# Optimization experiments

Hardware: AMD Instinct MI355X
Metric: run time of the kernel (lower is better)

The kernel has to match this reference:

```python
import jax, jax.numpy as jnp
import numpy as np


def _ln(x, g, b, eps=1e-6):
    m = jnp.mean(x, axis=-1, keepdims=True)
    v = jnp.mean((x - m) ** 2, axis=-1, keepdims=True)
    return g * (x - m) * jax.lax.rsqrt(v + eps) + b


def setup_inputs() -> dict:
    key = jax.random.key(0)
    ks = jax.random.split(key, 18)
    B, T, F, K = 4, 2048, 128, 1          # batch, seq, raw features, time2vec kernel size
    D = F * (K + 2)                        # 384 = d_model after time2vec concat
    H, HS, FF = 8, 128, 512                # heads, head_size, ff_dim
    s = 0.02
    inp = {
        "x":    jax.random.normal(ks[0], (B, T, F), jnp.float32),
        # Time2Vec params
        "wb":   jax.random.uniform(ks[1], (F,), jnp.float32, -0.05, 0.05),
        "bb":   jax.random.uniform(ks[2], (F,), jnp.float32, -0.05, 0.05),
        "wa":   jax.random.uniform(ks[3], (F, K), jnp.float32, -0.05, 0.05),
        "ba":   jax.random.uniform(ks[4], (F, K), jnp.float32, -0.05, 0.05),
        # MHA params (per-head kernels, as in the addons layer)
        "Wq":   jax.random.normal(ks[5], (H, D, HS), jnp.float32) * s,
        "Wk":   jax.random.normal(ks[6], (H, D, HS), jnp.float32) * s,
        "Wv":   jax.random.normal(ks[7], (H, D, HS), jnp.float32) * s,
        "Wp":   jax.random.normal(ks[8], (H, HS, D), jnp.float32) * s,
        "bp":   jnp.zeros((D,), jnp.float32),
        "ln1_g": jnp.ones((D,), jnp.float32),
        "ln1_b": jnp.zeros((D,), jnp.float32),
        # FFN (Conv1D kernel_size=1 == dense over channels)
        "W1":   jax.random.normal(ks[9], (D, FF), jnp.float32) * s,
        "b1":   jnp.zeros((FF,), jnp.float32),
        "W2":   jax.random.normal(ks[10], (FF, D), jnp.float32) * s,
        "b2":   jnp.zeros((D,), jnp.float32),
        "ln2_g": jnp.ones((D,), jnp.float32),
        "ln2_b": jnp.zeros((D,), jnp.float32),
    }
    return inp


def reference(x, wb, bb, wa, ba, Wq, Wk, Wv, Wp, bp, ln1_g, ln1_b,
              W1, b1, W2, b2, ln2_g, ln2_b):
    B, T, F = x.shape
    # ---- Time2Vec (applied per timestep) ----
    bias = wb * x + bb                                        # [B,T,F]
    dp = jnp.einsum('btf,fk->btk', x, wa)[:, :, None, :] + ba # [B,T,F,K]
    wgts = jnp.sin(dp)
    t2v = jnp.concatenate([bias[..., None], wgts], axis=-1).reshape(B, T, -1)
    h = jnp.concatenate([x, t2v], axis=-1)                    # [B,T,D]

    # ---- MultiHeadAttention (self-attention, eval: dropout=0) ----
    HS = Wq.shape[-1]
    q = jnp.einsum('bni,hio->bnho', h, Wq) / jnp.sqrt(jnp.asarray(HS, h.dtype))
    k = jnp.einsum('bmi,hio->bmho', h, Wk)
    v = jnp.einsum('bmi,hio->bmho', h, Wv)
    logits = jnp.einsum('bnho,bmho->bhnm', q, k)              # [B,H,T,T]
    attn = jax.nn.softmax(logits, axis=-1)
    mo = jnp.einsum('bhnm,bmhi->bnhi', attn, v)               # [B,T,H,HS]
    a = jnp.einsum('bnhi,hio->bno', mo, Wp) + bp              # [B,T,D]

    h1 = _ln(h + a, ln1_g, ln1_b)
    # ---- FFN (Conv1D ks=1 -> dense) ----
    f = jax.nn.relu(jnp.einsum('btd,df->btf', h1, W1) + b1)
    f = jnp.einsum('btf,fd->btd', f, W2) + b2
    h2 = _ln(h1 + f, ln2_g, ln2_b)

    return h2.reshape(B, -1)                                  # [B, T*D]
```

## Files before the change

### kernel.cpp

```cpp
#include <hip/hip_runtime.h>
#include <hip/hip_bf16.h>

typedef __hip_bfloat16 bf16;
typedef __attribute__((ext_vector_type(8))) short short8;
typedef __attribute__((ext_vector_type(4))) short short4v;
typedef __attribute__((ext_vector_type(4))) float floatx4;

#define B_  4
#define T_  2048
#define F_  128
#define D_  384
#define H_  8
#define HS_ 128
#define FF_ 512
#define NT_ (B_*T_)

__device__ __forceinline__ float b2f(bf16 v) { return __bfloat162float(v); }
__device__ __forceinline__ bf16  f2b(float v) { return __float2bfloat16(v); }
__device__ __forceinline__ unsigned short f2bu(float f) {
    bf16 b = __float2bfloat16(f);
    union { bf16 h; unsigned short u; } cv; cv.h = b; return cv.u;
}

__device__ __forceinline__ float ldin(const void* p, size_t i, int f32) {
    return f32 ? ((const float*)p)[i] : b2f(((const bf16*)p)[i]);
}

__global__ void k_detect(const void* __restrict__ x, int* __restrict__ flag)
{
    if (threadIdx.x == 0 && blockIdx.x == 0) {
        const unsigned short* u = (const unsigned short*)x;
        int big = 0;
        for (int i = 0; i < 128; i++) {
            int e = (u[i] >> 7) & 0xFF;
            if (e >= 141) big++;
        }
        *flag = (big >= 8) ? 1 : 0;
    }
}

__global__ void k_pack_all(const void* __restrict__ Wq, const void* __restrict__ Wk,
                           const void* __restrict__ Wv, const void* __restrict__ Wp,
                           const void* __restrict__ bp, const void* __restrict__ W1,
                           const void* __restrict__ b1, const void* __restrict__ W2,
                           const void* __restrict__ b2, bf16* __restrict__ wbase,
                           const int* __restrict__ dtf, int mode1)
{
    const int f32 = *dtf;
    int idx = blockIdx.x * 256 + threadIdx.x;
    if (idx < 1179648) {
        int k = idx % D_;
        int head, mat, ch;
        if (mode1) {
            int n = idx / D_;
            mat = n >> 10; int w = n & 1023; head = w >> 7; ch = w & 127;
        } else {
            int n = (idx / D_) % 1536; int rnd = idx / (D_ * 1536);
            mat = n >> 9; int w = n & 511; head = rnd * 4 + (w >> 7); ch = w & 127;
        }
        const void* W = (mat == 0 ? Wq : (mat == 1 ? Wk : Wv));
        float v = ldin(W, (size_t)head * D_ * HS_ + (size_t)k * HS_ + ch, f32);
        if (mat == 0) v *= 0.08838834764831845f;
        wbase[idx] = f2b(v);
    } else if (idx < 1572864) {
        int l = idx - 1179648; int o = l >> 10, c = l & 1023;
        wbase[idx] = f2b(ldin(Wp, (size_t)c * D_ + o, f32));
    } else if (idx < 1769472) {
        int l = idx - 1572864; int d = l % D_, f = l / D_;
        wbase[idx] = f2b(ldin(W1, (size_t)d * FF_ + f, f32));
    } else if (idx < 1966080) {
        int l = idx - 1769472; int ff = l % FF_, d = l / FF_;
        wbase[idx] = f2b(ldin(W2, (size_t)ff * D_ + d, f32));
    } else if (idx < 1968896) {
        int l = idx - 1966080;
        float bv = 0.f;
        if (l >= 2432)      bv = ldin(b2, l - 2432, f32);
        else if (l >= 1920) bv = ldin(b1, l - 1920, f32);
        else if (l >= 1536) bv = ldin(bp, l - 1536, f32);
        wbase[idx] = f2b(bv);
    }
}

__global__ void k_t2v(const void* __restrict__ x, const void* __restrict__ wb,
                      const void* __restrict__ bb, const void* __restrict__ wa,
                      const void* __restrict__ ba, bf16* __restrict__ h,
                      const int* __restrict__ dtf)
{
    const int f32 = *dtf;
    int row = blockIdx.x;
    int f = threadIdx.x;
    float xv = ldin(x, (size_t)row * F_ + f, f32);
    float prod = xv * ldin(wa, f, f32);
    #pragma unroll
    for (int off = 32; off; off >>= 1) prod += __shfl_down(prod, off, 64);
    __shared__ float sdot[2];
    if ((threadIdx.x & 63) == 0) sdot[threadIdx.x >> 6] = prod;
    __syncthreads();
    float dot = sdot[0] + sdot[1];

    float bias = ldin(wb, f, f32) * xv + ldin(bb, f, f32);
    float sn   = sinf(dot + ldin(ba, f, f32));
    bf16* hr = h + (size_t)row * D_;
    hr[f]            = f2b(xv);
    hr[F_ + 2*f]     = f2b(bias);
    hr[F_ + 2*f + 1] = f2b(sn);
}

template<bool BIAS, bool RELU>
__global__ __launch_bounds__(256) void
k_gemm_mfma(const bf16* __restrict__ A, const bf16* __restrict__ Wt,
            const bf16* __restrict__ bias, bf16* __restrict__ C,
            int K, int N)
{
    __shared__ __align__(16) bf16 As[128][72];
    __shared__ __align__(16) bf16 Bs[128][72];

    const int tid  = threadIdx.x;
    const int wave = tid >> 6;
    const int lane = tid & 63;
    const int r    = lane & 15;
    const int g    = lane >> 4;
    const int rh   = (wave & 1) * 64;
    const int chh  = (wave >> 1) * 64;
    const int row0 = blockIdx.x * 128;
    const int col0 = blockIdx.y * 128;

    floatx4 acc[4][4];
    #pragma unroll
    for (int mt = 0; mt < 4; mt++)
        #pragma unroll
        for (int nt = 0; nt < 4; nt++) acc[mt][nt] = (floatx4){0.f,0.f,0.f,0.f};

    for (int k0 = 0; k0 < K; k0 += 64) {
        #pragma unroll
        for (int s = 0; s < 4; s++) {
            int i = tid + s * 256;
            int row = i >> 3, c8 = i & 7;
            *(uint4*)&As[row][c8 * 8] =
                *(const uint4*)(A + (size_t)(row0 + row) * K + k0 + c8 * 8);
            *(uint4*)&Bs[row][c8 * 8] =
                *(const uint4*)(Wt + (size_t)(col0 + row) * K + k0 + c8 * 8);
        }
        __syncthreads();
        #pragma unroll
        for (int ks = 0; ks < 2; ks++) {
            short8 af[4], bf[4];
            #pragma unroll
            for (int mt = 0; mt < 4; mt++)
                af[mt] = *(const short8*)&As[rh + mt * 16 + r][ks * 32 + g * 8];
            #pragma unroll
            for (int nt = 0; nt < 4; nt++)
                bf[nt] = *(const short8*)&Bs[chh + nt * 16 + r][ks * 32 + g * 8];
            #pragma unroll
            for (int mt = 0; mt < 4; mt++)
                #pragma unroll
                for (int nt = 0; nt < 4; nt++)
                    acc[mt][nt] = __builtin_amdgcn_mfma_f32_16x16x32_bf16(
                        af[mt], bf[nt], acc[mt][nt], 0, 0, 0);
        }
        __syncthreads();
    }

    #pragma unroll
    for (int mt = 0; mt < 4; mt++) {
        #pragma unroll
        for (int nt = 0; nt < 4; nt++) {
            int col = col0 + chh + nt * 16 + r;
            float bv = BIAS ? b2f(bias[col]) : 0.f;
            #pragma unroll
            for (int reg = 0; reg < 4; reg++) {
                int row = row0 + rh + mt * 16 + 4 * g + reg;
                float v = acc[mt][nt][reg] + bv;
                if (RELU) v = fmaxf(v, 0.f);
                C[(size_t)row * N + col] = f2b(v);
            }
        }
    }
}

#define ATM 128
#define ATN 64
__global__ __launch_bounds__(256) void
k_attn_mfma(const bf16* __restrict__ cqkv, bf16* __restrict__ mo,
            int stride, int koff, int voff, int head_base)
{
    __shared__ __align__(16) bf16 Ks[64][136];
    __shared__ __align__(16) bf16 Vt[128 * 64];
    __shared__ __align__(16) bf16 Pb[4][32][72];

    const int tid  = threadIdx.x;
    const int wave = tid >> 6;
    const int lane = tid & 63;
    const int r    = lane & 15;
    const int g    = lane >> 4;

    const int combo = blockIdx.x;
    const int hh = combo >> 2, b = combo & 3;
    const int t0 = blockIdx.y * ATM;
    const int head = head_base + hh;

    const bf16* qb = cqkv + ((size_t)(b * T_ + t0)) * stride + hh * 128;
    const bf16* kb = cqkv + ((size_t)(b * T_)) * stride + koff + hh * 128;
    const bf16* vb = cqkv + ((size_t)(b * T_)) * stride + voff + hh * 128;

    short8 qfrag[2][4];
    #pragma unroll
    for (int mt = 0; mt < 2; mt++)
        #pragma unroll
        for (int ks = 0; ks < 4; ks++)
            qfrag[mt][ks] = *(const short8*)(qb +
                (size_t)(wave * 32 + mt * 16 + r) * stride + ks * 32 + g * 8);

    const int kv4 = tid & 15, oct = tid >> 4;
    uint4 kreg[4], vreg[4];
    #pragma unroll
    for (int s = 0; s < 4; s++) {
        int i = tid + s * 256;
        kreg[s] = *(const uint4*)(kb + (size_t)(i >> 4) * stride + (i & 15) * 8);
        vreg[s] = *(const uint4*)(vb + (size_t)(kv4 * 4 + s) * stride + oct * 8);
    }

    floatx4 O[2][8];
    #pragma unroll
    for (int mt = 0; mt < 2; mt++)
        #pragma unroll
        for (int dt = 0; dt < 8; dt++) O[mt][dt] = (floatx4){0.f, 0.f, 0.f, 0.f};
    float l_run[2] = {0.f, 0.f};

    for (int m0 = 0; m0 < T_; m0 += ATN) {
        __syncthreads();
        #pragma unroll
        for (int s = 0; s < 4; s++) {
            int i = tid + s * 256;
            *(uint4*)&Ks[i >> 4][(i & 15) * 8] = kreg[s];
        }
        {
            const unsigned short* u0 = (const unsigned short*)&vreg[0];
            const unsigned short* u1 = (const unsigned short*)&vreg[1];
            const unsigned short* u2 = (const unsigned short*)&vreg[2];
            const unsigned short* u3 = (const unsigned short*)&vreg[3];
            #pragma unroll
            for (int j = 0; j < 8; j++) {
                short4v w4 = { (short)u0[j], (short)u1[j], (short)u2[j], (short)u3[j] };
                int d = oct * 8 + j;
                *(short4v*)&Vt[d * 64 + ((kv4 * 4) ^ (j * 8))] = w4;
            }
        }
        __syncthreads();
        if (m0 + ATN < T_) {
            #pragma unroll
            for (int s = 0; s < 4; s++) {
                int i = tid + s * 256;
                kreg[s] = *(const uint4*)(kb + (size_t)(m0 + ATN + (i >> 4)) * stride + (i & 15) * 8);
                vreg[s] = *(const uint4*)(vb + (size_t)(m0 + ATN + kv4 * 4 + s) * stride + oct * 8);
            }
        }

        floatx4 sacc[2][4];
        #pragma unroll
        for (int mt = 0; mt < 2; mt++)
            #pragma unroll
            for (int t = 0; t < 4; t++) sacc[mt][t] = (floatx4){0.f,0.f,0.f,0.f};
        #pragma unroll
        for (int t = 0; t < 4; t++) {
            #pragma unroll
            for (int ks = 0; ks < 4; ks++) {
                short8 kf = *(const short8*)&Ks[t * 16 + r][ks * 32 + g * 8];
                sacc[0][t] = __builtin_amdgcn_mfma_f32_16x16x32_bf16(kf, qfrag[0][ks], sacc[0][t], 0, 0, 0);
                sacc[1][t] = __builtin_amdgcn_mfma_f32_16x16x32_bf16(kf, qfrag[1][ks], sacc[1][t], 0, 0, 0);
            }
        }

        #pragma unroll
        for (int mt = 0; mt < 2; mt++) {
            float tsum = 0.f;
            #pragma unroll
            for (int t = 0; t < 4; t++) {
                short4v pw;
                #pragma unroll
                for (int reg = 0; reg < 4; reg++) {
                    float p = __expf(sacc[mt][t][reg]);
                    tsum += p;
                    pw[reg] = (short)f2bu(p);
                }
                *(short4v*)&Pb[wave][mt * 16 + r][t * 16 + 4 * g] = pw;
            }
            tsum += __shfl_xor(tsum, 16);
            tsum += __shfl_xor(tsum, 32);
            l_run[mt] += tsum;
        }
        asm volatile("s_waitcnt lgkmcnt(0)" ::: "memory");

        const int sw = (r & 7) * 8;
        #pragma unroll
        for (int ks = 0; ks < 2; ks++) {
            short8 pf0 = *(const short8*)&Pb[wave][0 * 16 + r][ks * 32 + g * 8];
            short8 pf1 = *(const short8*)&Pb[wave][1 * 16 + r][ks * 32 + g * 8];
            #pragma unroll
            for (int dt = 0; dt < 8; dt++) {
                int d = dt * 16 + r;
                short8 vf = *(const short8*)&Vt[d * 64 + ((ks * 32 + 8 * g) ^ sw)];
                O[0][dt] = __builtin_amdgcn_mfma_f32_16x16x32_bf16(pf0, vf, O[0][dt], 0, 0, 0);
                O[1][dt] = __builtin_amdgcn_mfma_f32_16x16x32_bf16(pf1, vf, O[1][dt], 0, 0, 0);
            }
        }
    }

    #pragma unroll
    for (int mt = 0; mt < 2; mt++) {
        float linv[4];
        #pragma unroll
        for (int reg = 0; reg < 4; reg++)
            linv[reg] = 1.f / __shfl(l_run[mt], 4 * g + reg);
        #pragma unroll
        for (int dt = 0; dt < 8; dt++) {
            #pragma unroll
            for (int reg = 0; reg < 4; reg++) {
                int t = t0 + wave * 32 + mt * 16 + 4 * g + reg;
                mo[(((size_t)(b * T_ + t)) * H_ + head) * HS_ + dt * 16 + r] =
                    f2b(O[mt][dt][reg] * linv[reg]);
            }
        }
    }
}

template<bool FINAL>
__global__ void k_ln(const bf16* __restrict__ in1, const bf16* __restrict__ in2,
                     const void* __restrict__ g, const void* __restrict__ be,
                     void* __restrict__ out, const int* __restrict__ dtf)
{
    const int f32 = *dtf;
    int row = blockIdx.x;
    int tid = threadIdx.x;
    size_t base = (size_t)row * D_;
    int c0 = tid, c1 = tid + 128, c2 = tid + 256;
    float x0 = b2f(in1[base + c0]) + b2f(in2[base + c0]);
    float x1 = b2f(in1[base + c1]) + b2f(in2[base + c1]);
    float x2 = b2f(in1[base + c2]) + b2f(in2[base + c2]);

    __shared__ float sb1[2], sb2[2];
    float s = x0 + x1 + x2;
    #pragma unroll
    for (int off = 32; off; off >>= 1) s += __shfl_down(s, off, 64);
    if ((tid & 63) == 0) sb1[tid >> 6] = s;
    __syncthreads();
    float m = (sb1[0] + sb1[1]) * (1.f / D_);

    float d0 = x0 - m, d1 = x1 - m, d2 = x2 - m;
    float sq = d0*d0 + d1*d1 + d2*d2;
    #pragma unroll
    for (int off = 32; off; off >>= 1) sq += __shfl_down(sq, off, 64);
    if ((tid & 63) == 0) sb2[tid >> 6] = sq;
    __syncthreads();
    float rstd = rsqrtf((sb2[0] + sb2[1]) * (1.f / D_) + 1e-6f);

    float y0 = ldin(g, c0, f32) * d0 * rstd + ldin(be, c0, f32);
    float y1 = ldin(g, c1, f32) * d1 * rstd + ldin(be, c1, f32);
    float y2 = ldin(g, c2, f32) * d2 * rstd + ldin(be, c2, f32);
    if (FINAL && f32) {
        float* o = (float*)out;
        o[base + c0] = y0; o[base + c1] = y1; o[base + c2] = y2;
    } else {
        bf16* o = (bf16*)out;
        o[base + c0] = f2b(y0); o[base + c1] = f2b(y1); o[base + c2] = f2b(y2);
    }
}

extern "C" void kernel_launch(void* const* d_in, const int* in_sizes, int n_in,
                              void* d_out, int out_size, void* d_ws, size_t ws_size,
                              hipStream_t stream)
{
    const void* x     = d_in[0];
    const void* wb    = d_in[1];
    const void* bb    = d_in[2];
    const void* wa    = d_in[3];
    const void* ba    = d_in[4];
    const void* Wq    = d_in[5];
    const void* Wk    = d_in[6];
    const void* Wv    = d_in[7];
    const void* Wp    = d_in[8];
    const void* bp    = d_in[9];
    const void* ln1_g = d_in[10];
    const void* ln1_b = d_in[11];
    const void* W1    = d_in[12];
    const void* b1    = d_in[13];
    const void* W2    = d_in[14];
    const void* b2    = d_in[15];
    const void* ln2_g = d_in[16];
    const void* ln2_b = d_in[17];

    const size_t NEED1 = (size_t)38669056 * 2 + 4;
    const int mode1 = (ws_size >= NEED1) ? 1 : 0;

    bf16* ws    = (bf16*)d_ws;
    bf16* h     = ws;
    bf16* cqkv  = h + 3145728;
    bf16* mo    = cqkv + (mode1 ? 25165824 : 12582912);
    bf16* wbase = mo + 8388608;
    bf16* wqkv  = wbase;
    bf16* wp    = wbase + 1179648;
    bf16* w1    = wbase + 1572864;
    bf16* w2    = wbase + 1769472;
    bf16* biasp = wbase + 1966080;
    int*  flag  = (int*)(wbase + 1968896);

    bf16* a  = cqkv;
    bf16* h1 = h;
    bf16* f  = cqkv + 3145728;
    bf16* f2 = cqkv + 7340032;

    k_detect<<<1, 64, 0, stream>>>(x, flag);

    k_pack_all<<<7691, 256, 0, stream>>>(Wq, Wk, Wv, Wp, bp, W1, b1, W2, b2,
                                         wbase, flag, mode1);

    k_t2v<<<NT_, 128, 0, stream>>>(x, wb, bb, wa, ba, h, flag);

    if (mode1) {
        dim3 gq(NT_ / 128, 3072 / 128);
        k_gemm_mfma<false, false><<<gq, 256, 0, stream>>>(h, wqkv, nullptr,
                                                          cqkv, D_, 3072);
        dim3 gatt(B_ * 8, T_ / ATM);
        k_attn_mfma<<<gatt, 256, 0, stream>>>(cqkv, mo, 3072, 1024, 2048, 0);
    } else {
        for (int round = 0; round < 2; round++) {
            dim3 gq(NT_ / 128, 1536 / 128);
            k_gemm_mfma<false, false><<<gq, 256, 0, stream>>>(
                h, wqkv + (size_t)round * 1536 * D_, nullptr, cqkv, D_, 1536);
            dim3 gatt(B_ * 4, T_ / ATM);
            k_attn_mfma<<<gatt, 256, 0, stream>>>(cqkv, mo, 1536, 512, 1024,
                                                  round * 4);
        }
    }

    dim3 gp(NT_ / 128, D_ / 128);
    k_gemm_mfma<true, false><<<gp, 256, 0, stream>>>(
        mo, wp, biasp + 1536, a, H_ * HS_, D_);

    k_ln<false><<<NT_, 128, 0, stream>>>(h, a, ln1_g, ln1_b, h1, flag);

    dim3 g1(NT_ / 128, FF_ / 128);
    k_gemm_mfma<true, true><<<g1, 256, 0, stream>>>(
        h1, w1, biasp + 1920, f, D_, FF_);

    dim3 g2(NT_ / 128, D_ / 128);
    k_gemm_mfma<true, false><<<g2, 256, 0, stream>>>(
        f, w2, biasp + 2432, f2, FF_, D_);

    k_ln<true><<<NT_, 128, 0, stream>>>(h1, f2, ln2_g, ln2_b, d_out, flag);
}
```

Baseline: 316.9 us.

## Split attention over two KV halves and merge partials inside projection GEMM

Adds a split-KV mode that launches the attention kernel with a third grid dimension. Each half of the key/value sequence writes unnormalized partial outputs and row sums, which doubles the block count so more of the device is busy. A new projection kernel merges the two partials while loading its A tile, normalizing by the summed row sums. The cost is extra workspace and global traffic for the partial buffers, plus a simpler, unpipelined projection GEMM. The mode runs only when the workspace is large enough.

```diff
diff --git a/kernel.cpp b/kernel.cpp
--- a/kernel.cpp
+++ b/kernel.cpp
@@ -178,26 +178,115 @@
     }
 }
 
-#define ATM 128
-#define ATN 64
 __global__ __launch_bounds__(256) void
-k_attn_mfma(const bf16* __restrict__ cqkv, bf16* __restrict__ mo,
-            int stride, int koff, int voff, int head_base)
-{
-    __shared__ __align__(16) bf16 Ks[64][136];
-    __shared__ __align__(16) bf16 Vt[128 * 64];
-    __shared__ __align__(16) bf16 Pb[4][32][72];
+k_proj_merge(const bf16* __restrict__ Op, const float* __restrict__ lp,
+             const bf16* __restrict__ Wt, const bf16* __restrict__ bias,
+             bf16* __restrict__ C)
+{
+    const int K = 1024, N = 384;
+    __shared__ __align__(16) bf16 As[128][72];
+    __shared__ __align__(16) bf16 Bs[128][72];
 
     const int tid  = threadIdx.x;
     const int wave = tid >> 6;
     const int lane = tid & 63;
     const int r    = lane & 15;
     const int g    = lane >> 4;
+    const int rh   = (wave & 1) * 64;
+    const int chh  = (wave >> 1) * 64;
+    const int row0 = blockIdx.x * 128;
+    const int col0 = blockIdx.y * 128;
+
+    floatx4 acc[4][4];
+    #pragma unroll
+    for (int mt = 0; mt < 4; mt++)
+        #pragma unroll
+        for (int nt = 0; nt < 4; nt++) acc[mt][nt] = (floatx4){0.f,0.f,0.f,0.f};
+
+    for (int k0 = 0; k0 < K; k0 += 64) {
+        #pragma unroll
+        for (int s = 0; s < 4; s++) {
+            int i = tid + s * 256;
+            int row = i >> 3, c8 = i & 7;
+            int R = row0 + row;
+            int kcol = k0 + c8 * 8;
+            int hidx = kcol >> 7;
+            float l0 = lp[(size_t)R * H_ + hidx];
+            float l1 = lp[(size_t)NT_ * H_ + (size_t)R * H_ + hidx];
+            float inv = 1.f / (l0 + l1);
+            uint4 p0 = *(const uint4*)(Op + (size_t)R * 1024 + kcol);
+            uint4 p1 = *(const uint4*)(Op + (size_t)NT_ * H_ * HS_ +
+                                       (size_t)R * 1024 + kcol);
+            const bf16* e0 = (const bf16*)&p0;
+            const bf16* e1 = (const bf16*)&p1;
+            bf16 tmp[8];
+            #pragma unroll
+            for (int j = 0; j < 8; j++)
+                tmp[j] = f2b((b2f(e0[j]) + b2f(e1[j])) * inv);
+            *(uint4*)&As[row][c8 * 8] = *(uint4*)tmp;
+            *(uint4*)&Bs[row][c8 * 8] =
+                *(const uint4*)(Wt + (size_t)(col0 + row) * K + k0 + c8 * 8);
+        }
+        __syncthreads();
+        #pragma unroll
+        for (int ks = 0; ks < 2; ks++) {
+            short8 af[4], bf[4];
+            #pragma unroll
+            for (int mt = 0; mt < 4; mt++)
+                af[mt] = *(const short8*)&As[rh + mt * 16 + r][ks * 32 + g * 8];
+            #pragma unroll
+            for (int nt = 0; nt < 4; nt++)
+                bf[nt] = *(const short8*)&Bs[chh + nt * 16 + r][ks * 32 + g * 8];
+            #pragma unroll
+            for (int mt = 0; mt < 4; mt++)
+                #pragma unroll
+                for (int nt = 0; nt < 4; nt++)
+                    acc[mt][nt] = __builtin_amdgcn_mfma_f32_16x16x32_bf16(
+                        af[mt], bf[nt], acc[mt][nt], 0, 0, 0);
+        }
+        __syncthreads();
+    }
+
+    #pragma unroll
+    for (int mt = 0; mt < 4; mt++) {
+        #pragma unroll
+        for (int nt = 0; nt < 4; nt++) {
+            int col = col0 + chh + nt * 16 + r;
+            float bv = b2f(bias[col]);
+            #pragma unroll
+            for (int reg = 0; reg < 4; reg++) {
+                int row = row0 + rh + mt * 16 + 4 * g + reg;
+                C[(size_t)row * N + col] = f2b(acc[mt][nt][reg] + bv);
+            }
+        }
+    }
+}
+
+#define ATM 128
+#define ATN 64
+template<bool SPLIT>
+__global__ __launch_bounds__(256) void
+k_attn_mfma(const bf16* __restrict__ cqkv, bf16* __restrict__ outp,
+            float* __restrict__ lp, int stride, int koff, int voff,
+            int head_base)
+{
+    __shared__ __align__(16) bf16 Ks[64][136];
+    __shared__ __align__(16) bf16 Vt[128 * 64];
+    __shared__ __align__(16) bf16 Pb[4][32][72];
+
+    const int tid  = threadIdx.x;
+    const int wave = tid >> 6;
+    const int lane = tid & 63;
+    const int r    = lane & 15;
+    const int g    = lane >> 4;
 
     const int combo = blockIdx.x;
     const int hh = combo >> 2, b = combo & 3;
     const int t0 = blockIdx.y * ATM;
     const int head = head_base + hh;
+    const int split = SPLIT ? blockIdx.z : 0;
+    const int kv0 = split * (T_ / 2);
+    const int kvN = SPLIT ? (T_ / 2) : T_;
 
     const bf16* qb = cqkv + ((size_t)(b * T_ + t0)) * stride + hh * 128;
     const bf16* kb = cqkv + ((size_t)(b * T_)) * stride + koff + hh * 128;
@@ -216,8 +305,8 @@
     #pragma unroll
     for (int s = 0; s < 4; s++) {
         int i = tid + s * 256;
-        kreg[s] = *(const uint4*)(kb + (size_t)(i >> 4) * stride + (i & 15) * 8);
-        vreg[s] = *(const uint4*)(vb + (size_t)(kv4 * 4 + s) * stride + oct * 8);
+        kreg[s] = *(const uint4*)(kb + (size_t)(kv0 + (i >> 4)) * stride + (i & 15) * 8);
+        vreg[s] = *(const uint4*)(vb + (size_t)(kv0 + kv4 * 4 + s) * stride + oct * 8);
     }
 
     floatx4 O[2][8];
@@ -227,7 +316,7 @@
         for (int dt = 0; dt < 8; dt++) O[mt][dt] = (floatx4){0.f, 0.f, 0.f, 0.f};
     float l_run[2] = {0.f, 0.f};
 
-    for (int m0 = 0; m0 < T_; m0 += ATN) {
+    for (int m0 = kv0; m0 < kv0 + kvN; m0 += ATN) {
         __syncthreads();
         #pragma unroll
         for (int s = 0; s < 4; s++) {
@@ -247,7 +336,7 @@
             }
         }
         __syncthreads();
-        if (m0 + ATN < T_) {
+        if (m0 + ATN < kv0 + kvN) {
             #pragma unroll
             for (int s = 0; s < 4; s++) {
                 int i = tid + s * 256;
@@ -306,19 +395,38 @@
         }
     }
 
-    #pragma unroll
-    for (int mt = 0; mt < 2; mt++) {
-        float linv[4];
-        #pragma unroll
-        for (int reg = 0; reg < 4; reg++)
-            linv[reg] = 1.f / __shfl(l_run[mt], 4 * g + reg);
-        #pragma unroll
-        for (int dt = 0; dt < 8; dt++) {
-            #pragma unroll
-            for (int reg = 0; reg < 4; reg++) {
-                int t = t0 + wave * 32 + mt * 16 + 4 * g + reg;
-                mo[(((size_t)(b * T_ + t)) * H_ + head) * HS_ + dt * 16 + r] =
-                    f2b(O[mt][dt][reg] * linv[reg]);
+    if (SPLIT) {
+        bf16* op = outp + (size_t)split * NT_ * H_ * HS_;
+        float* lps = lp + (size_t)split * NT_ * H_;
+        #pragma unroll
+        for (int mt = 0; mt < 2; mt++) {
+            if (g == 0)
+                lps[((size_t)(b * T_ + t0 + wave * 32 + mt * 16 + r)) * H_ + head] = l_run[mt];
+            #pragma unroll
+            for (int dt = 0; dt < 8; dt++) {
+                #pragma unroll
+                for (int reg = 0; reg < 4; reg++) {
+                    int t = t0 + wave * 32 + mt * 16 + 4 * g + reg;
+                    op[(((size_t)(b * T_ + t)) * H_ + head) * HS_ + dt * 16 + r] =
+                        f2b(O[mt][dt][reg]);
+                }
+            }
+        }
+    } else {
+        #pragma unroll
+        for (int mt = 0; mt < 2; mt++) {
+            float linv[4];
+            #pragma unroll
+            for (int reg = 0; reg < 4; reg++)
+                linv[reg] = 1.f / __shfl(l_run[mt], 4 * g + reg);
+            #pragma unroll
+            for (int dt = 0; dt < 8; dt++) {
+                #pragma unroll
+                for (int reg = 0; reg < 4; reg++) {
+                    int t = t0 + wave * 32 + mt * 16 + 4 * g + reg;
+                    outp[(((size_t)(b * T_ + t)) * H_ + head) * HS_ + dt * 16 + r] =
+                        f2b(O[mt][dt][reg] * linv[reg]);
+                }
             }
         }
     }
@@ -389,14 +497,29 @@
     const void* ln2_g = d_in[16];
     const void* ln2_b = d_in[17];
 
+    const size_t NEED2 = (size_t)47319810 * 2 + 4;
     const size_t NEED1 = (size_t)38669056 * 2 + 4;
-    const int mode1 = (ws_size >= NEED1) ? 1 : 0;
+    const int mode2 = (ws_size >= NEED2) ? 1 : 0;
+    const int mode1 = (!mode2 && ws_size >= NEED1) ? 1 : 0;
 
     bf16* ws    = (bf16*)d_ws;
     bf16* h     = ws;
     bf16* cqkv  = h + 3145728;
-    bf16* mo    = cqkv + (mode1 ? 25165824 : 12582912);
-    bf16* wbase = mo + 8388608;
+    bf16*  mo    = nullptr;
+    bf16*  Opart = nullptr;
+    float* lpart = nullptr;
+    bf16*  wbase;
+    if (mode2) {
+        Opart = cqkv + 25165824;
+        lpart = (float*)(Opart + 16777216);
+        wbase = Opart + 16777216 + 262144;
+    } else if (mode1) {
+        mo    = cqkv + 25165824;
+        wbase = mo + 8388608;
+    } else {
+        mo    = cqkv + 12582912;
+        wbase = mo + 8388608;
+    }
     bf16* wqkv  = wbase;
     bf16* wp    = wbase + 1179648;
     bf16* w1    = wbase + 1572864;
@@ -412,30 +535,43 @@
     k_detect<<<1, 64, 0, stream>>>(x, flag);
 
     k_pack_all<<<7691, 256, 0, stream>>>(Wq, Wk, Wv, Wp, bp, W1, b1, W2, b2,
-                                         wbase, flag, mode1);
+                                         wbase, flag, mode2 || mode1);
 
     k_t2v<<<NT_, 128, 0, stream>>>(x, wb, bb, wa, ba, h, flag);
 
-    if (mode1) {
+    if (mode2) {
+        dim3 gq(NT_ / 128, 3072 / 128);
+        k_gemm_mfma<false, false><<<gq, 256, 0, stream>>>(h, wqkv, nullptr,
+                                                          cqkv, D_, 3072);
+        dim3 gatt(B_ * 8, T_ / ATM, 2);
+        k_attn_mfma<true><<<gatt, 256, 0, stream>>>(cqkv, Opart, lpart,
+                                                    3072, 1024, 2048, 0);
+        dim3 gp(NT_ / 128, D_ / 128);
+        k_proj_merge<<<gp, 256, 0, stream>>>(Opart, lpart, wp, biasp + 1536, a);
+    } else if (mode1) {
         dim3 gq(NT_ / 128, 3072 / 128);
         k_gemm_mfma<false, false><<<gq, 256, 0, stream>>>(h, wqkv, nullptr,
                                                           cqkv, D_, 3072);
         dim3 gatt(B_ * 8, T_ / ATM);
-        k_attn_mfma<<<gatt, 256, 0, stream>>>(cqkv, mo, 3072, 1024, 2048, 0);
+        k_attn_mfma<false><<<gatt, 256, 0, stream>>>(cqkv, mo, nullptr,
+                                                     3072, 1024, 2048, 0);
+        dim3 gp(NT_ / 128, D_ / 128);
+        k_gemm_mfma<true, false><<<gp, 256, 0, stream>>>(
+            mo, wp, biasp + 1536, a, H_ * HS_, D_);
     } else {
         for (int round = 0; round < 2; round++) {
             dim3 gq(NT_ / 128, 1536 / 128);
             k_gemm_mfma<false, false><<<gq, 256, 0, stream>>>(
                 h, wqkv + (size_t)round * 1536 * D_, nullptr, cqkv, D_, 1536);
             dim3 gatt(B_ * 4, T_ / ATM);
-            k_attn_mfma<<<gatt, 256, 0, stream>>>(cqkv, mo, 1536, 512, 1024,
-                                                  round * 4);
-        }
-    }
-
-    dim3 gp(NT_ / 128, D_ / 128);
-    k_gemm_mfma<true, false><<<gp, 256, 0, stream>>>(
-        mo, wp, biasp + 1536, a, H_ * HS_, D_);
+            k_attn_mfma<false><<<gatt, 256, 0, stream>>>(cqkv, mo, nullptr,
+                                                         1536, 512, 1024,
+                                                         round * 4);
+        }
+        dim3 gp(NT_ / 128, D_ / 128);
+        k_gemm_mfma<true, false><<<gp, 256, 0, stream>>>(
+            mo, wp, biasp + 1536, a, H_ * HS_, D_);
+    }
 
     k_ln<false><<<NT_, 128, 0, stream>>>(h, a, ln1_g, ln1_b, h1, flag);
 
```

Result: slower. 327.9 us (+3.5%).

## Use direct global-to-LDS loads and XOR-swizzled shared layouts in GEMM and attention

Applied to the files above, without the earlier changes.

The GEMM tile loads now use global_load_lds, which writes 16-byte chunks straight into LDS without staging them in registers. The padded row layouts are replaced by unpadded buffers with an XOR swizzle to avoid bank conflicts, and the attention K and P buffers get the same swizzle. The sync is moved to the top of the k-loop. This cuts register traffic and LDS footprint. The risk is that 16-byte global_load_lds needs hardware support, and the kernel now relies on the swizzle and LDS placement being exactly right.

```diff
diff --git a/kernel.cpp b/kernel.cpp
--- a/kernel.cpp
+++ b/kernel.cpp
@@ -20,6 +20,12 @@
 __device__ __forceinline__ unsigned short f2bu(float f) {
     bf16 b = __float2bfloat16(f);
     union { bf16 h; unsigned short u; } cv; cv.h = b; return cv.u;
+}
+
+__device__ __forceinline__ void gld16(const bf16* g, bf16* l) {
+    __builtin_amdgcn_global_load_lds(
+        (const __attribute__((address_space(1))) void*)g,
+        (__attribute__((address_space(3))) void*)l, 16, 0, 0);
 }
 
 __device__ __forceinline__ float ldin(const void* p, size_t i, int f32) {
@@ -112,14 +118,15 @@
             const bf16* __restrict__ bias, bf16* __restrict__ C,
             int K, int N)
 {
-    __shared__ __align__(16) bf16 As[128][72];
-    __shared__ __align__(16) bf16 Bs[128][72];
+    __shared__ __align__(16) bf16 As[128 * 64];
+    __shared__ __align__(16) bf16 Bs[128 * 64];
 
     const int tid  = threadIdx.x;
     const int wave = tid >> 6;
     const int lane = tid & 63;
     const int r    = lane & 15;
     const int g    = lane >> 4;
+    const int sw   = (r & 7) * 8;
     const int rh   = (wave & 1) * 64;
     const int chh  = (wave >> 1) * 64;
     const int row0 = blockIdx.x * 128;
@@ -132,14 +139,14 @@
         for (int nt = 0; nt < 4; nt++) acc[mt][nt] = (floatx4){0.f,0.f,0.f,0.f};
 
     for (int k0 = 0; k0 < K; k0 += 64) {
+        __syncthreads();
         #pragma unroll
         for (int s = 0; s < 4; s++) {
             int i = tid + s * 256;
-            int row = i >> 3, c8 = i & 7;
-            *(uint4*)&As[row][c8 * 8] =
-                *(const uint4*)(A + (size_t)(row0 + row) * K + k0 + c8 * 8);
-            *(uint4*)&Bs[row][c8 * 8] =
-                *(const uint4*)(Wt + (size_t)(col0 + row) * K + k0 + c8 * 8);
+            int row = i >> 3;
+            int gcol = ((i & 7) * 8) ^ ((row & 7) * 8);
+            gld16(A  + (size_t)(row0 + row) * K + k0 + gcol, As + (size_t)i * 8);
+            gld16(Wt + (size_t)(col0 + row) * K + k0 + gcol, Bs + (size_t)i * 8);
         }
         __syncthreads();
         #pragma unroll
@@ -147,10 +154,12 @@
             short8 af[4], bf[4];
             #pragma unroll
             for (int mt = 0; mt < 4; mt++)
-                af[mt] = *(const short8*)&As[rh + mt * 16 + r][ks * 32 + g * 8];
+                af[mt] = *(const short8*)&As[(rh + mt * 16 + r) * 64 +
+                                             ((ks * 32 + g * 8) ^ sw)];
             #pragma unroll
             for (int nt = 0; nt < 4; nt++)
-                bf[nt] = *(const short8*)&Bs[chh + nt * 16 + r][ks * 32 + g * 8];
+                bf[nt] = *(const short8*)&Bs[(chh + nt * 16 + r) * 64 +
+                                             ((ks * 32 + g * 8) ^ sw)];
             #pragma unroll
             for (int mt = 0; mt < 4; mt++)
                 #pragma unroll
@@ -158,7 +167,6 @@
                     acc[mt][nt] = __builtin_amdgcn_mfma_f32_16x16x32_bf16(
                         af[mt], bf[nt], acc[mt][nt], 0, 0, 0);
         }
-        __syncthreads();
     }
 
     #pragma unroll
@@ -181,18 +189,19 @@
 #define ATM 128
 #define ATN 64
 __global__ __launch_bounds__(256) void
-k_attn_mfma(const bf16* __restrict__ cqkv, bf16* __restrict__ mo,
+k_attn_mfma(const bf16* __restrict__ cqkv, bf16* __restrict__ outp,
             int stride, int koff, int voff, int head_base)
 {
-    __shared__ __align__(16) bf16 Ks[64][136];
+    __shared__ __align__(16) bf16 Ks[64 * 128];
     __shared__ __align__(16) bf16 Vt[128 * 64];
-    __shared__ __align__(16) bf16 Pb[4][32][72];
+    __shared__ __align__(16) bf16 Pb[4][32 * 64];
 
     const int tid  = threadIdx.x;
     const int wave = tid >> 6;
     const int lane = tid & 63;
     const int r    = lane & 15;
     const int g    = lane >> 4;
+    const int sw   = (r & 7) * 8;
 
     const int combo = blockIdx.x;
     const int hh = combo >> 2, b = combo & 3;
@@ -232,7 +241,8 @@
         #pragma unroll
         for (int s = 0; s < 4; s++) {
             int i = tid + s * 256;
-            *(uint4*)&Ks[i >> 4][(i & 15) * 8] = kreg[s];
+            int row = i >> 4, col = (i & 15) * 8;
+            *(uint4*)&Ks[row * 128 + (col ^ ((row & 7) * 8))] = kreg[s];
         }
         {
             const unsigned short* u0 = (const unsigned short*)&vreg[0];
@@ -265,7 +275,8 @@
         for (int t = 0; t < 4; t++) {
             #pragma unroll
             for (int ks = 0; ks < 4; ks++) {
-                short8 kf = *(const short8*)&Ks[t * 16 + r][ks * 32 + g * 8];
+                short8 kf = *(const short8*)&Ks[(t * 16 + r) * 128 +
+                                                ((ks * 32 + g * 8) ^ sw)];
                 sacc[0][t] = __builtin_amdgcn_mfma_f32_16x16x32_bf16(kf, qfrag[0][ks], sacc[0][t], 0, 0, 0);
                 sacc[1][t] = __builtin_amdgcn_mfma_f32_16x16x32_bf16(kf, qfrag[1][ks], sacc[1][t], 0, 0, 0);
             }
@@ -283,7 +294,8 @@
                     tsum += p;
                     pw[reg] = (short)f2bu(p);
                 }
-                *(short4v*)&Pb[wave][mt * 16 + r][t * 16 + 4 * g] = pw;
+                *(short4v*)&Pb[wave][(mt * 16 + r) * 64 +
+                                     ((t * 16 + 4 * g) ^ sw)] = pw;
             }
             tsum += __shfl_xor(tsum, 16);
             tsum += __shfl_xor(tsum, 32);
@@ -291,11 +303,12 @@
         }
         asm volatile("s_waitcnt lgkmcnt(0)" ::: "memory");
 
-        const int sw = (r & 7) * 8;
         #pragma unroll
         for (int ks = 0; ks < 2; ks++) {
-            short8 pf0 = *(const short8*)&Pb[wave][0 * 16 + r][ks * 32 + g * 8];
-            short8 pf1 = *(const short8*)&Pb[wave][1 * 16 + r][ks * 32 + g * 8];
+            short8 pf0 = *(const short8*)&Pb[wave][(0 * 16 + r) * 64 +
+                                                   ((ks * 32 + g * 8) ^ sw)];
+            short8 pf1 = *(const short8*)&Pb[wave][(1 * 16 + r) * 64 +
+                                                   ((ks * 32 + g * 8) ^ sw)];
             #pragma unroll
             for (int dt = 0; dt < 8; dt++) {
                 int d = dt * 16 + r;
@@ -317,7 +330,7 @@
             #pragma unroll
             for (int reg = 0; reg < 4; reg++) {
                 int t = t0 + wave * 32 + mt * 16 + 4 * g + reg;
-                mo[(((size_t)(b * T_ + t)) * H_ + head) * HS_ + dt * 16 + r] =
+                outp[(((size_t)(b * T_ + t)) * H_ + head) * HS_ + dt * 16 + r] =
                     f2b(O[mt][dt][reg] * linv[reg]);
             }
         }
```

After: 359.7 us. 13.5% more time.
